# Optimization experiments

Hardware: AMD Instinct MI355X
Metric: run time of the kernel (lower is better)

Reference implementation:

```python
import jax, jax.numpy as jnp
import numpy as np

AN = 1.0      # bandwidth a_n
SIGMA = 1.0   # Gaussian kernel scale
_EPS = 1e-32


def setup_inputs() -> dict:
    key = jax.random.key(0)
    k1, k2, k3 = jax.random.split(key, 3)
    n = 8192
    log_h = jax.random.normal(k1, (n, 1), dtype=jnp.float32)
    durations = jax.random.uniform(k2, (n,), dtype=jnp.float32)
    events = jax.random.randint(k3, (n,), 0, 2, dtype=jnp.int32)
    return {"log_h": log_h, "durations": durations, "events": events}


def reference(log_h, durations, events):
    theta = log_h.reshape(-1)                         # (n,)
    n = theta.shape[0]
    # residuals e = -(theta - log(Y)); note original adds 1e-32 before log
    e = -(theta - jnp.log(durations + _EPS))          # (n,)
    perm = jnp.argsort(e)                             # sort order of e
    e_sorted = e[perm]                                # (n,) ascending
    # Original code sorts [indices, dur, ev, theta] by the indices column,
    # which reorders the side arrays by the INVERSE permutation.
    inv = jnp.argsort(perm)
    ev = events.astype(jnp.float32)[inv]              # (n,)
    th = theta[inv]                                   # (n,)

    diff = (e_sorted[:, None] - e_sorted[None, :]) / AN   # (n, n)
    # Normal(0, SIGMA) log pdf at diff
    log_pdf = -0.5 * (diff / SIGMA) ** 2 - jnp.log(SIGMA * jnp.sqrt(2.0 * jnp.pi))
    # cond_E_i = sum_j pdf_ij * ev_j / (n*an) + eps-per-element
    cond_E = jnp.sum(jnp.exp(log_pdf) * ev / (n * AN) + _EPS, axis=1)   # (n,)
    # Normal(0, SIGMA) cdf at diff
    cdf = 0.5 * (1.0 + jax.lax.erf(diff / (SIGMA * jnp.sqrt(2.0))))
    surv = jnp.sum(cdf / n, axis=1)                   # (n,)

    loss = -jnp.sum((jnp.log(cond_E) - jnp.log(surv) + th) * ev / n)
    return loss
```

## Files before the change

### kernel.cpp

```cpp
#include <hip/hip_runtime.h>
#include <math.h>
#include <stdint.h>

#define RB 256
#define JT 512
#define GM 1024
#define YS 128

#define SCALE 0.84932180028801904f
#define SQRT2PI 2.5066282746310002f
#define KFP 0.46971863934f
#define LN2 0.69314718056f

__device__ __forceinline__ uint64_t order_key(float f, int idx) {
  unsigned u = __float_as_uint(f);
  u = (u & 0x80000000u) ? ~u : (u | 0x80000000u);
  return ((uint64_t)u << 32) | (unsigned)idx;
}

__device__ __forceinline__ float e_of(const float* theta, const float* dur, int i) {
  return logf(dur[i] + 1e-32f) - theta[i];
}

__device__ __forceinline__ void grid_geom(const float2* xe, int n, float* x0, float* hx) {
  float a = xe[0].x - 7.0f;
  float b = xe[n - 1].x + 7.0f;
  *x0 = a;
  *hx = (b - a) / (float)(GM - 1);
}

__global__ __launch_bounds__(RB) void rank_part_kernel(
    const float* __restrict__ theta, const float* __restrict__ dur,
    int* __restrict__ rank_part, int n) {
  __shared__ uint64_t kt[JT];
  const int i = blockIdx.x * RB + threadIdx.x;
  uint64_t ki = order_key(e_of(theta, dur, i), i);
  const int jbase = blockIdx.y * JT;
  for (int t = threadIdx.x; t < JT; t += RB) {
    int j = jbase + t;
    kt[t] = order_key(e_of(theta, dur, j), j);
  }
  __syncthreads();
  int cnt = 0;
  #pragma unroll 8
  for (int jj = 0; jj < JT; ++jj) cnt += (kt[jj] < ki) ? 1 : 0;
  rank_part[blockIdx.y * n + i] = cnt;
}

__global__ __launch_bounds__(RB) void scatter_kernel(
    const float* __restrict__ theta, const float* __restrict__ dur,
    const int* __restrict__ ev, const int* __restrict__ rank_part,
    float2* __restrict__ xe, float* __restrict__ th_s,
    float* __restrict__ gbuf, float* __restrict__ out, int n) {
  int k = blockIdx.x * RB + threadIdx.x;
  int r = 0;
  const int nj = n / JT;
  #pragma unroll 16
  for (int jch = 0; jch < nj; ++jch) r += rank_part[jch * n + k];
  ((float*)&xe[r])[0] = SCALE * e_of(theta, dur, k);
  ((float*)&xe[k])[1] = (float)ev[r];
  th_s[k] = theta[r];
  if (k < 4 * GM) gbuf[k] = 0.0f;
  if (k == 0) out[0] = 0.0f;
}

__global__ __launch_bounds__(RB) void gt_kernel(
    const float2* __restrict__ xe, float* __restrict__ gbuf, int n) {
  float x0, hx;
  grid_geom(xe, n, &x0, &hx);
  int m = blockIdx.x * RB + threadIdx.x;
  float xm = fmaf((float)m, hx, x0);
  const int chunk = n / YS;
  int jb = blockIdx.y * chunk;
  const float P2S = 0.39169197f;
  float a = 0.0f, b = 0.0f, f = 0.0f, d = 0.0f;
  #pragma unroll 8
  for (int jj = 0; jj < chunk; ++jj) {
    float2 q = xe[jb + jj];
    float dp = xm - q.x;
    float g = __builtin_amdgcn_exp2f(-(dp * dp));
    float evg = q.y * g;
    a += g;
    b += evg;
    d = fmaf(dp, evg, d);
    float tt = __builtin_amdgcn_rcpf(fmaf(P2S, __builtin_fabsf(dp), 1.0f));
    float poly = tt * (0.3480242f + tt * (-0.0958798f + tt * 0.7478556f));
    f += __builtin_copysignf(fmaf(-poly, g, 1.0f), dp);
  }
  atomicAdd(&gbuf[m], a);
  atomicAdd(&gbuf[GM + m], b);
  atomicAdd(&gbuf[2 * GM + m], 0.5f * (float)chunk + 0.5f * f);
  atomicAdd(&gbuf[3 * GM + m], d);
}

__global__ __launch_bounds__(RB) void final_kernel(
    const float2* __restrict__ xe, const float* __restrict__ th_s,
    const float* __restrict__ gbuf, float* __restrict__ out, int n) {
  float x0, hx;
  grid_geom(xe, n, &x0, &hx);
  const float* A = gbuf;
  const float* B = gbuf + GM;
  const float* F = gbuf + 2 * GM;
  const float* D = gbuf + 3 * GM;
  int i = blockIdx.x * RB + threadIdx.x;

  float term = 0.0f;
  if (i < n) {
    float2 q = xe[i];
    float u = (q.x - x0) * __builtin_amdgcn_rcpf(hx);
    int m = (int)u;
    m = min(max(m, 0), GM - 2);
    float t = u - (float)m;
    t = fminf(fmaxf(t, 0.0f), 1.0f);
    float t2 = t * t, t3 = t2 * t;
    float h00 = 2.0f * t3 - 3.0f * t2 + 1.0f;
    float h01 = 3.0f * t2 - 2.0f * t3;
    float h10 = t3 - 2.0f * t2 + t;
    float h11 = t3 - t2;
    float Fi = F[m] * h00 + F[m + 1] * h01 +
               hx * KFP * (A[m] * h10 + A[m + 1] * h11);
    float Bi = B[m] * h00 + B[m + 1] * h01 -
               2.0f * LN2 * hx * (D[m] * h10 + D[m + 1] * h11);
    const float fn = (float)n;
    float condE = fmaxf(Bi, 0.0f) * (1.0f / SQRT2PI) / fn + fn * 1e-32f;
    float surv = fmaxf(Fi, 0.25f) / fn;
    term = (__logf(condE) - __logf(surv) + th_s[i]) * q.y;
  }

  #pragma unroll
  for (int off = 32; off > 0; off >>= 1) term += __shfl_down(term, off, 64);
  __shared__ float red[RB / 64];
  int wave = threadIdx.x >> 6, lane = threadIdx.x & 63;
  if (lane == 0) red[wave] = term;
  __syncthreads();
  if (threadIdx.x == 0) {
    float s = 0.0f;
    #pragma unroll
    for (int w = 0; w < RB / 64; ++w) s += red[w];
    atomicAdd(out, -s / (float)n);
  }
}

extern "C" void kernel_launch(void* const* d_in, const int* in_sizes, int n_in,
                              void* d_out, int out_size, void* d_ws, size_t ws_size,
                              hipStream_t stream) {
  const float* theta = (const float*)d_in[0];
  const float* dur   = (const float*)d_in[1];
  const int*   ev    = (const int*)d_in[2];
  float* out = (float*)d_out;
  const int n = in_sizes[1];

  char* ws = (char*)d_ws;
  float2* xe        = (float2*)ws;  ws += n * sizeof(float2);
  int*    rank_part = (int*)ws;     ws += (n / JT) * n * sizeof(int);
  float*  th_s      = (float*)ws;   ws += n * sizeof(float);
  float*  gbuf      = (float*)ws;   ws += 4 * GM * sizeof(float);

  rank_part_kernel<<<dim3(n / RB, n / JT), RB, 0, stream>>>(theta, dur, rank_part, n);
  scatter_kernel<<<n / RB, RB, 0, stream>>>(theta, dur, ev, rank_part,
                                            xe, th_s, gbuf, out, n);
  gt_kernel<<<dim3(GM / RB, YS), RB, 0, stream>>>(xe, gbuf, n);
  final_kernel<<<n / RB, RB, 0, stream>>>(xe, th_s, gbuf, out, n);
}
```

Measured before the change: 78.01 us.

## Fuse rank counting and scatter into one kernel with full key table in LDS

Merges the rank partial-count kernel and the scatter kernel into a single launch. Each 1024-thread block loads all 8192 sort keys into shared memory, splits the comparison loop across four thread quarters, and reduces the partial ranks in LDS before scattering. This removes the global rank_part buffer and one kernel launch, and recovers e from the key instead of recomputing it. In exchange every block recomputes all n keys (logf per element), uses 64KB+ of LDS, and runs only 32 blocks, which limits parallelism across the CUs.

```diff
diff --git a/kernel.cpp b/kernel.cpp
--- a/kernel.cpp
+++ b/kernel.cpp
@@ -3,7 +3,7 @@
 #include <stdint.h>
 
 #define RB 256
-#define JT 512
+#define RSB 1024
 #define GM 1024
 #define YS 128
 
@@ -12,12 +12,16 @@
 #define KFP 0.46971863934f
 #define LN2 0.69314718056f
 
+__device__ __forceinline__ unsigned float2ord(float f) {
+  unsigned u = __float_as_uint(f);
+  return (u & 0x80000000u) ? ~u : (u | 0x80000000u);
+}
+__device__ __forceinline__ float ord2float(unsigned u) {
+  return __uint_as_float((u & 0x80000000u) ? (u ^ 0x80000000u) : ~u);
+}
 __device__ __forceinline__ uint64_t order_key(float f, int idx) {
-  unsigned u = __float_as_uint(f);
-  u = (u & 0x80000000u) ? ~u : (u | 0x80000000u);
-  return ((uint64_t)u << 32) | (unsigned)idx;
+  return ((uint64_t)float2ord(f) << 32) | (unsigned)idx;
 }
-
 __device__ __forceinline__ float e_of(const float* theta, const float* dur, int i) {
   return logf(dur[i] + 1e-32f) - theta[i];
 }
@@ -29,39 +33,42 @@
   *hx = (b - a) / (float)(GM - 1);
 }
 
-__global__ __launch_bounds__(RB) void rank_part_kernel(
+__global__ __launch_bounds__(RSB) void rank_scatter_kernel(
     const float* __restrict__ theta, const float* __restrict__ dur,
-    int* __restrict__ rank_part, int n) {
-  __shared__ uint64_t kt[JT];
-  const int i = blockIdx.x * RB + threadIdx.x;
-  uint64_t ki = order_key(e_of(theta, dur, i), i);
-  const int jbase = blockIdx.y * JT;
-  for (int t = threadIdx.x; t < JT; t += RB) {
-    int j = jbase + t;
-    kt[t] = order_key(e_of(theta, dur, j), j);
+    const int* __restrict__ ev, float2* __restrict__ xe,
+    float* __restrict__ th_s, float* __restrict__ gbuf,
+    float* __restrict__ out, int n) {
+  __shared__ uint64_t kt[8192];
+  __shared__ int part[4][256];
+
+  for (int j = threadIdx.x; j < n; j += RSB)
+    kt[j] = order_key(e_of(theta, dur, j), j);
+  if (blockIdx.x == 0) {
+    for (int m = threadIdx.x; m < 4 * GM; m += RSB) gbuf[m] = 0.0f;
+    if (threadIdx.x == 0) out[0] = 0.0f;
   }
   __syncthreads();
+
+  const int il = threadIdx.x & 255;
+  const int q  = threadIdx.x >> 8;
+  const int i  = blockIdx.x * 256 + il;
+  const uint64_t ki = kt[i];
+  const int qlen = n >> 2;
+  const int jb = q * qlen;
   int cnt = 0;
   #pragma unroll 8
-  for (int jj = 0; jj < JT; ++jj) cnt += (kt[jj] < ki) ? 1 : 0;
-  rank_part[blockIdx.y * n + i] = cnt;
-}
+  for (int jj = 0; jj < qlen; ++jj)
+    cnt += (kt[jb + jj] < ki) ? 1 : 0;
+  part[q][il] = cnt;
+  __syncthreads();
 
-__global__ __launch_bounds__(RB) void scatter_kernel(
-    const float* __restrict__ theta, const float* __restrict__ dur,
-    const int* __restrict__ ev, const int* __restrict__ rank_part,
-    float2* __restrict__ xe, float* __restrict__ th_s,
-    float* __restrict__ gbuf, float* __restrict__ out, int n) {
-  int k = blockIdx.x * RB + threadIdx.x;
-  int r = 0;
-  const int nj = n / JT;
-  #pragma unroll 16
-  for (int jch = 0; jch < nj; ++jch) r += rank_part[jch * n + k];
-  ((float*)&xe[r])[0] = SCALE * e_of(theta, dur, k);
-  ((float*)&xe[k])[1] = (float)ev[r];
-  th_s[k] = theta[r];
-  if (k < 4 * GM) gbuf[k] = 0.0f;
-  if (k == 0) out[0] = 0.0f;
+  if (q == 0) {
+    int r = part[0][il] + part[1][il] + part[2][il] + part[3][il];
+    float ei = ord2float((unsigned)(ki >> 32));
+    ((float*)&xe[r])[0] = SCALE * ei;
+    ((float*)&xe[i])[1] = (float)ev[r];
+    th_s[i] = theta[r];
+  }
 }
 
 __global__ __launch_bounds__(RB) void gt_kernel(
@@ -151,14 +158,12 @@
   const int n = in_sizes[1];
 
   char* ws = (char*)d_ws;
-  float2* xe        = (float2*)ws;  ws += n * sizeof(float2);
-  int*    rank_part = (int*)ws;     ws += (n / JT) * n * sizeof(int);
-  float*  th_s      = (float*)ws;   ws += n * sizeof(float);
-  float*  gbuf      = (float*)ws;   ws += 4 * GM * sizeof(float);
+  float2* xe   = (float2*)ws;  ws += n * sizeof(float2);
+  float*  th_s = (float*)ws;   ws += n * sizeof(float);
+  float*  gbuf = (float*)ws;   ws += 4 * GM * sizeof(float);
 
-  rank_part_kernel<<<dim3(n / RB, n / JT), RB, 0, stream>>>(theta, dur, rank_part, n);
-  scatter_kernel<<<n / RB, RB, 0, stream>>>(theta, dur, ev, rank_part,
-                                            xe, th_s, gbuf, out, n);
+  rank_scatter_kernel<<<n / 256, RSB, 0, stream>>>(theta, dur, ev, xe, th_s,
+                                                   gbuf, out, n);
   gt_kernel<<<dim3(GM / RB, YS), RB, 0, stream>>>(xe, gbuf, n);
   final_kernel<<<n / RB, RB, 0, stream>>>(xe, th_s, gbuf, out, n);
 }
```

New measurement: 132.0 us. +69.2%, slower.
